# Optimization experiments

Measured on AMD Instinct MI355X. Metric: run time of the kernel, lower is better.

Reference implementation:

```python
import jax, jax.numpy as jnp
import numpy as np

B, C, H, W = 8, 128, 64, 64
GROUPS = 8
EPS = 1e-5


def setup_inputs() -> dict:
    key = jax.random.key(0)
    ks = jax.random.split(key, 4)
    x = jax.random.normal(ks[0], (B, C, H, W), dtype=jnp.float32)
    gamma = jnp.ones((C,), jnp.float32)
    beta = jnp.zeros((C,), jnp.float32)
    w_qkv = jax.random.normal(ks[1], (3 * C, C), jnp.float32) * (C ** -0.5)
    b_qkv = jnp.zeros((3 * C,), jnp.float32)
    w_proj = jax.random.normal(ks[2], (C, C), jnp.float32) * (C ** -0.5)
    b_proj = jnp.zeros((C,), jnp.float32)
    return {"x": x, "gamma": gamma, "beta": beta, "w_qkv": w_qkv,
            "b_qkv": b_qkv, "w_proj": w_proj, "b_proj": b_proj}


def group_norm(x, gamma, beta):
    b, c, h, w = x.shape
    xg = x.reshape(b, GROUPS, c // GROUPS, h, w)
    mean = xg.mean(axis=(2, 3, 4), keepdims=True)
    var = xg.var(axis=(2, 3, 4), keepdims=True)
    xn = ((xg - mean) * jax.lax.rsqrt(var + EPS)).reshape(b, c, h, w)
    return xn * gamma[None, :, None, None] + beta[None, :, None, None]


def reference(x, gamma, beta, w_qkv, b_qkv, w_proj, b_proj):
    b, c, h, w = x.shape
    n = h * w
    hn = group_norm(x, gamma, beta)
    # 1x1 conv == channel matmul
    qkv = jnp.einsum('oc,bchw->bohw', w_qkv, hn) + b_qkv[None, :, None, None]
    q, k, v = jnp.split(qkv.reshape(b, 3 * c, n), 3, axis=1)  # each [b,c,n]
    attn = jax.nn.softmax(jnp.einsum('bci,bcj->bij', q, k) * (c ** -0.5), axis=-1)
    out = jnp.einsum('bij,bcj->bci', attn, v).reshape(b, c, h, w)
    proj = jnp.einsum('oc,bchw->bohw', w_proj, out) + b_proj[None, :, None, None]
    return x + proj
```

## Files before the change

kernel.cpp:

```cpp
#include <hip/hip_runtime.h>
#include <cstdint>

#define NB 8
#define NC 128
#define NPIX 4096
#define NGROUP 8
#define CPG 16
#define EPS_GN 1e-5f
#define QSCALE 0.12751879523604132f
#define NSPLIT 2
#define JTILES (NPIX / 64 / NSPLIT)

typedef __attribute__((ext_vector_type(8))) short short8;
typedef __attribute__((ext_vector_type(16))) float f32x16;

typedef __attribute__((address_space(1))) const void gvoid_t;
typedef __attribute__((address_space(3))) void svoid_t;

__device__ __forceinline__ unsigned packbf(float lo, float hi) {
  unsigned r;
  asm("v_cvt_pk_bf16_f32 %0, %1, %2" : "=v"(r) : "v"(lo), "v"(hi));
  return r;
}

__device__ __forceinline__ int swK(int row) {
  return ((row & 7) << 1) | ((row >> 3) & 1);
}

__global__ __launch_bounds__(256) void k_gn_stats(const float* __restrict__ x,
                                                  float* __restrict__ stats) {
  int blk = blockIdx.x;
  const float4* base = (const float4*)(x + (size_t)blk * CPG * NPIX);
  float s = 0.f, ss = 0.f;
  for (int i = threadIdx.x; i < CPG * NPIX / 4; i += 256) {
    float4 v = base[i];
    s  += v.x + v.y + v.z + v.w;
    ss += v.x * v.x + v.y * v.y + v.z * v.z + v.w * v.w;
  }
#pragma unroll
  for (int off = 32; off >= 1; off >>= 1) {
    s  += __shfl_down(s, off);
    ss += __shfl_down(ss, off);
  }
  __shared__ float red[8];
  int wid = threadIdx.x >> 6;
  if ((threadIdx.x & 63) == 0) { red[wid] = s; red[4 + wid] = ss; }
  __syncthreads();
  if (threadIdx.x == 0) {
    float S  = red[0] + red[1] + red[2] + red[3];
    float SS = red[4] + red[5] + red[6] + red[7];
    float mean = S * (1.f / (CPG * NPIX));
    float var  = SS * (1.f / (CPG * NPIX)) - mean * mean;
    stats[blk * 2]     = mean;
    stats[blk * 2 + 1] = rsqrtf(var + EPS_GN);
  }
}

__global__ __launch_bounds__(256) void k_qkv(const float* __restrict__ x,
                                             const float* __restrict__ stats,
                                             const float* __restrict__ gamma,
                                             const float* __restrict__ beta,
                                             const float* __restrict__ w,
                                             const float* __restrict__ bias,
                                             ushort* __restrict__ qT,
                                             ushort* __restrict__ kT,
                                             ushort* __restrict__ vB) {
  __shared__ ushort At[128 * 128];
  __shared__ ushort Bt[128 * 128];
  __shared__ float sArr[128], tArr[128], biasS[384];
  int b = blockIdx.x, pt = blockIdx.y;
  int p0 = pt * 128;
  int tid = threadIdx.x;
  if (tid < 128) {
    int g = tid >> 4;
    float mean = stats[(b * NGROUP + g) * 2];
    float rstd = stats[(b * NGROUP + g) * 2 + 1];
    float sc = rstd * gamma[tid];
    sArr[tid] = sc;
    tArr[tid] = beta[tid] - mean * sc;
  }
  for (int i = tid; i < 384; i += 256) biasS[i] = bias[i];
  __syncthreads();
  const float* xb = x + (size_t)b * NC * NPIX;
#pragma unroll
  for (int u = 0; u < 8; ++u) {
    int task = tid + u * 256;
    int p = task & 127, cc = task >> 7;
    int c0 = cc * 8;
    float v[8];
#pragma unroll
    for (int i = 0; i < 8; ++i)
      v[i] = sArr[c0 + i] * xb[(size_t)(c0 + i) * NPIX + p0 + p] + tArr[c0 + i];
    uint4 pk;
    pk.x = packbf(v[0], v[1]); pk.y = packbf(v[2], v[3]);
    pk.z = packbf(v[4], v[5]); pk.w = packbf(v[6], v[7]);
    *(uint4*)&Bt[((p << 4) + (cc ^ (p & 7))) << 3] = pk;
  }
  int lane = tid & 63, wv = tid >> 6;
  int lq = lane & 31, h = lane >> 5;

  for (int ot = 0; ot < 3; ++ot) {
    __syncthreads();
#pragma unroll
    for (int u = 0; u < 8; ++u) {
      int task = tid + u * 256;
      int o = task >> 4, cc = task & 15;
      const float* wp = w + ((size_t)(ot * 128 + o)) * 128 + cc * 8;
      float4 a = *(const float4*)wp;
      float4 bq = *(const float4*)(wp + 4);
      uint4 pk;
      pk.x = packbf(a.x, a.y);  pk.y = packbf(a.z, a.w);
      pk.z = packbf(bq.x, bq.y); pk.w = packbf(bq.z, bq.w);
      *(uint4*)&At[((o << 4) + (cc ^ (o & 7))) << 3] = pk;
    }
    __syncthreads();
    short8 af[8];
    int arow = wv * 32 + lq;
#pragma unroll
    for (int kk = 0; kk < 8; ++kk) {
      int ch = kk * 2 + h;
      af[kk] = *(const short8*)&At[((arow << 4) + (ch ^ (arow & 7))) << 3];
    }
#pragma unroll
    for (int np = 0; np < 2; ++np) {
      int nt0 = np * 2, nt1 = np * 2 + 1;
      int br0 = nt0 * 32 + lq, br1 = nt1 * 32 + lq;
      f32x16 a0, a1;
#pragma unroll
      for (int r = 0; r < 16; ++r) { a0[r] = 0.f; a1[r] = 0.f; }
      __builtin_amdgcn_s_setprio(1);
#pragma unroll
      for (int kk = 0; kk < 8; ++kk) {
        int ch = kk * 2 + h;
        short8 h0 = *(const short8*)&Bt[((br0 << 4) + (ch ^ (br0 & 7))) << 3];
        short8 h1 = *(const short8*)&Bt[((br1 << 4) + (ch ^ (br1 & 7))) << 3];
        a0 = __builtin_amdgcn_mfma_f32_32x32x16_bf16(af[kk], h0, a0, 0, 0, 0);
        a1 = __builtin_amdgcn_mfma_f32_32x32x16_bf16(af[kk], h1, a1, 0, 0, 0);
      }
      __builtin_amdgcn_s_setprio(0);
#pragma unroll
      for (int half = 0; half < 2; ++half) {
        f32x16& acc = half ? a1 : a0;
        int pg = p0 + (half ? nt1 : nt0) * 32 + lq;
        if (ot < 2) {
          ushort* dst = (ot == 0) ? qT : kT;
          float sc = (ot == 0) ? QSCALE : 1.0f;
#pragma unroll
          for (int g2 = 0; g2 < 4; ++g2) {
            int orow = wv * 32 + 4 * h + 8 * g2;
            uint2 st;
            st.x = packbf((acc[g2 * 4 + 0] + biasS[ot * 128 + orow + 0]) * sc,
                          (acc[g2 * 4 + 1] + biasS[ot * 128 + orow + 1]) * sc);
            st.y = packbf((acc[g2 * 4 + 2] + biasS[ot * 128 + orow + 2]) * sc,
                          (acc[g2 * 4 + 3] + biasS[ot * 128 + orow + 3]) * sc);
            *(uint2*)&dst[(((size_t)b << 12) + pg) * 128 + orow] = st;
          }
        } else {
#pragma unroll
          for (int r = 0; r < 16; ++r) {
            int orow = wv * 32 + (r & 3) + 8 * (r >> 2) + 4 * h;
            float vv = acc[r] + biasS[256 + orow];
            vB[((size_t)(b * 128 + orow) << 12) + pg] = (ushort)(packbf(vv, vv) & 0xffffu);
          }
        }
      }
    }
  }
}

__device__ __forceinline__ void stage_dma(const ushort* __restrict__ kT,
                                          const ushort* __restrict__ vB,
                                          ushort* lds, int bufsel, int b, int j0,
                                          int wid, int lane) {
  ushort* base = lds + bufsel * 16384;
#pragma unroll
  for (int u = 0; u < 4; ++u) {
    int g = u * 4 + wid;
    int id = g * 64 + lane;
    int row = id >> 4, ch = id & 15;
    const ushort* src = kT + (((size_t)b << 12) + j0 + row) * 128 + ((ch ^ swK(row)) << 3);
    ushort* dst = base + g * 512;
    __builtin_amdgcn_global_load_lds((gvoid_t*)src, (svoid_t*)dst, 16, 0, 0);
  }
#pragma unroll
  for (int u = 0; u < 4; ++u) {
    int g = u * 4 + wid;
    int id = g * 64 + lane;
    int row = id >> 3, ch = id & 7;
    const ushort* src = vB + (((size_t)(b * 128 + row)) << 12) + j0 + ((ch ^ (row & 7)) << 3);
    ushort* dst = base + 8192 + g * 512;
    __builtin_amdgcn_global_load_lds((gvoid_t*)src, (svoid_t*)dst, 16, 0, 0);
  }
}

__global__ __launch_bounds__(256, 2) void k_attn(const ushort* __restrict__ qT,
                                                 const ushort* __restrict__ kT,
                                                 const ushort* __restrict__ vB,
                                                 float* __restrict__ attP,
                                                 float2* __restrict__ mlv) {
  __shared__ ushort lds[32768];
  int tid = threadIdx.x;
  int b = blockIdx.x, qt = blockIdx.y, s = blockIdx.z;
  int wid = tid >> 6;
  int lane = tid & 63;
  int lq = lane & 31;
  int h = lane >> 5;
  int q0 = qt * 128 + wid * 32;
  int jbase = s * (NPIX / NSPLIT);

  short8 qf[8];
  const ushort* qp = qT + (((size_t)b << 12) + q0 + lq) * 128 + h * 8;
#pragma unroll
  for (int kk = 0; kk < 8; ++kk) qf[kk] = *(const short8*)(qp + kk * 16);

  f32x16 pacc[4];
#pragma unroll
  for (int nt = 0; nt < 4; ++nt)
#pragma unroll
    for (int r = 0; r < 16; ++r) pacc[nt][r] = 0.f;
  float m_run = -1e30f, l_run = 0.f;

  stage_dma(kT, vB, lds, 0, b, jbase, wid, lane);

  for (int t = 0; t < JTILES; ++t) {
    __syncthreads();
    if (t + 1 < JTILES)
      stage_dma(kT, vB, lds, (t + 1) & 1, b, jbase + ((t + 1) << 6), wid, lane);
    const ushort* cur = lds + (t & 1) * 16384;

    f32x16 s0, s1;
#pragma unroll
    for (int r = 0; r < 16; ++r) { s0[r] = 0.f; s1[r] = 0.f; }
    __builtin_amdgcn_s_setprio(1);
#pragma unroll
    for (int kk = 0; kk < 8; ++kk) {
      int ch = (kk << 1) + h;
      int r0 = lq;
      int r1 = 32 + lq;
      short8 kf0 = *(const short8*)&cur[((r0 << 4) + (ch ^ swK(r0))) << 3];
      short8 kf1 = *(const short8*)&cur[((r1 << 4) + (ch ^ swK(r1))) << 3];
      s0 = __builtin_amdgcn_mfma_f32_32x32x16_bf16(kf0, qf[kk], s0, 0, 0, 0);
      s1 = __builtin_amdgcn_mfma_f32_32x32x16_bf16(kf1, qf[kk], s1, 0, 0, 0);
    }
    __builtin_amdgcn_s_setprio(0);

    float tm[8];
#pragma unroll
    for (int r = 0; r < 8; ++r)
      tm[r] = fmaxf(fmaxf(s0[2 * r], s0[2 * r + 1]), fmaxf(s1[2 * r], s1[2 * r + 1]));
    float tmax = fmaxf(fmaxf(fmaxf(tm[0], tm[1]), fmaxf(tm[2], tm[3])),
                       fmaxf(fmaxf(tm[4], tm[5]), fmaxf(tm[6], tm[7])));
    tmax = fmaxf(tmax, __shfl_xor(tmax, 32));

    bool noresc = __all(tmax - m_run <= 8.f);
    float mcur = noresc ? m_run : fmaxf(m_run, tmax);

    float sum = 0.f;
#pragma unroll
    for (int r = 0; r < 16; ++r) { s0[r] = exp2f(s0[r] - mcur); sum += s0[r]; }
#pragma unroll
    for (int r = 0; r < 16; ++r) { s1[r] = exp2f(s1[r] - mcur); sum += s1[r]; }
    sum += __shfl_xor(sum, 32);

    if (noresc) {
      l_run += sum;
    } else {
      float alpha = exp2f(m_run - mcur);
      m_run = mcur;
      l_run = l_run * alpha + sum;
#pragma unroll
      for (int r = 0; r < 16; ++r) {
        int qr = (r & 3) + ((r >> 2) << 3) + (h << 2);
        float av = __shfl(alpha, qr);
        pacc[0][r] *= av; pacc[1][r] *= av; pacc[2][r] *= av; pacc[3][r] *= av;
      }
    }

    short8 pa[4];
#pragma unroll
    for (int kk = 0; kk < 4; ++kk) {
      float v0, v1, v2, v3, v4, v5, v6, v7;
      if (kk == 0)      { v0=s0[0];v1=s0[1];v2=s0[2];v3=s0[3];v4=s0[4];v5=s0[5];v6=s0[6];v7=s0[7]; }
      else if (kk == 1) { v0=s0[8];v1=s0[9];v2=s0[10];v3=s0[11];v4=s0[12];v5=s0[13];v6=s0[14];v7=s0[15]; }
      else if (kk == 2) { v0=s1[0];v1=s1[1];v2=s1[2];v3=s1[3];v4=s1[4];v5=s1[5];v6=s1[6];v7=s1[7]; }
      else              { v0=s1[8];v1=s1[9];v2=s1[10];v3=s1[11];v4=s1[12];v5=s1[13];v6=s1[14];v7=s1[15]; }
      unsigned P0a = packbf(v0, v1), P0b = packbf(v2, v3);
      unsigned P1a = packbf(v4, v5), P1b = packbf(v6, v7);
      unsigned sA = h ? P0a : P1a, sB = h ? P0b : P1b;
      unsigned rA = (unsigned)__shfl_xor((int)sA, 32);
      unsigned rB = (unsigned)__shfl_xor((int)sB, 32);
      uint4 wv;
      wv.x = h ? rA : P0a;  wv.y = h ? rB : P0b;
      wv.z = h ? P1a : rA;  wv.w = h ? P1b : rB;
      pa[kk] = __builtin_bit_cast(short8, wv);
    }

    __builtin_amdgcn_s_setprio(1);
#pragma unroll
    for (int nt = 0; nt < 4; ++nt) {
      int row = (nt << 5) + lq;
#pragma unroll
      for (int kk = 0; kk < 4; ++kk) {
        int ch = (kk << 1) + h;
        short8 vf = *(const short8*)&cur[8192 + (((row << 3) + (ch ^ (row & 7))) << 3)];
        pacc[nt] = __builtin_amdgcn_mfma_f32_32x32x16_bf16(pa[kk], vf, pacc[nt], 0, 0, 0);
      }
    }
    __builtin_amdgcn_s_setprio(0);
  }

  size_t sb = (size_t)(s * NB + b);
#pragma unroll
  for (int r = 0; r < 16; ++r) {
    int qr = (r & 3) + ((r >> 2) << 3) + (h << 2);
    size_t rowbase = (((sb << 12) + q0 + qr) << 7) + lq;
    attP[rowbase]      = pacc[0][r];
    attP[rowbase + 32] = pacc[1][r];
    attP[rowbase + 64] = pacc[2][r];
    attP[rowbase + 96] = pacc[3][r];
  }
  if (h == 0) {
    mlv[(sb << 12) + q0 + lq] = make_float2(m_run, l_run);
  }
}

__global__ __launch_bounds__(256) void k_proj(const float* __restrict__ x,
                                              const float* __restrict__ attP,
                                              const float2* __restrict__ mlv,
                                              const float* __restrict__ w,
                                              const float* __restrict__ bias,
                                              float* __restrict__ out) {
  __shared__ ushort At[128 * 128];
  __shared__ ushort Bt[128 * 128];
  __shared__ float c0s[128], c1s[128], biasS[128];
  int b = blockIdx.x, pt = blockIdx.y;
  int p0 = pt * 128;
  int tid = threadIdx.x;
  if (tid < 128) {
    float2 ml0 = mlv[(((size_t)b) << 12) + p0 + tid];
    float2 ml1 = mlv[(((size_t)(NB + b)) << 12) + p0 + tid];
    float M = fmaxf(ml0.x, ml1.x);
    float e0 = exp2f(ml0.x - M), e1 = exp2f(ml1.x - M);
    float inv = 1.f / (ml0.y * e0 + ml1.y * e1);
    c0s[tid] = e0 * inv;
    c1s[tid] = e1 * inv;
    biasS[tid] = bias[tid];
  }
  __syncthreads();
#pragma unroll
  for (int u = 0; u < 8; ++u) {
    int task = tid + u * 256;
    int p = task & 127, cc = task >> 7;
    const float* a0 = attP + ((((size_t)b << 12) + p0 + p) << 7) + cc * 8;
    const float* a1 = attP + ((((size_t)(NB + b) << 12) + p0 + p) << 7) + cc * 8;
    float c0 = c0s[p], c1 = c1s[p];
    float v[8];
    float4 x0 = *(const float4*)a0, x0b = *(const float4*)(a0 + 4);
    float4 x1 = *(const float4*)a1, x1b = *(const float4*)(a1 + 4);
    v[0] = x0.x * c0 + x1.x * c1;  v[1] = x0.y * c0 + x1.y * c1;
    v[2] = x0.z * c0 + x1.z * c1;  v[3] = x0.w * c0 + x1.w * c1;
    v[4] = x0b.x * c0 + x1b.x * c1; v[5] = x0b.y * c0 + x1b.y * c1;
    v[6] = x0b.z * c0 + x1b.z * c1; v[7] = x0b.w * c0 + x1b.w * c1;
    uint4 pk;
    pk.x = packbf(v[0], v[1]); pk.y = packbf(v[2], v[3]);
    pk.z = packbf(v[4], v[5]); pk.w = packbf(v[6], v[7]);
    *(uint4*)&Bt[((p << 4) + (cc ^ (p & 7))) << 3] = pk;
  }
#pragma unroll
  for (int u = 0; u < 8; ++u) {
    int task = tid + u * 256;
    int o = task >> 4, cc = task & 15;
    const float* wp = w + (size_t)o * 128 + cc * 8;
    float4 a = *(const float4*)wp;
    float4 bq = *(const float4*)(wp + 4);
    uint4 pk;
    pk.x = packbf(a.x, a.y);  pk.y = packbf(a.z, a.w);
    pk.z = packbf(bq.x, bq.y); pk.w = packbf(bq.z, bq.w);
    *(uint4*)&At[((o << 4) + (cc ^ (o & 7))) << 3] = pk;
  }
  __syncthreads();
  int lane = tid & 63, wv = tid >> 6;
  int lq = lane & 31, h = lane >> 5;
  short8 af[8];
  int arow = wv * 32 + lq;
#pragma unroll
  for (int kk = 0; kk < 8; ++kk) {
    int ch = kk * 2 + h;
    af[kk] = *(const short8*)&At[((arow << 4) + (ch ^ (arow & 7))) << 3];
  }
  const float* xb = x + (size_t)b * NC * NPIX;
  float* ob = out + (size_t)b * NC * NPIX;
#pragma unroll
  for (int np = 0; np < 2; ++np) {
    int nt0 = np * 2, nt1 = np * 2 + 1;
    int br0 = nt0 * 32 + lq, br1 = nt1 * 32 + lq;
    f32x16 a0, a1;
#pragma unroll
    for (int r = 0; r < 16; ++r) { a0[r] = 0.f; a1[r] = 0.f; }
    __builtin_amdgcn_s_setprio(1);
#pragma unroll
    for (int kk = 0; kk < 8; ++kk) {
      int ch = kk * 2 + h;
      short8 h0 = *(const short8*)&Bt[((br0 << 4) + (ch ^ (br0 & 7))) << 3];
      short8 h1 = *(const short8*)&Bt[((br1 << 4) + (ch ^ (br1 & 7))) << 3];
      a0 = __builtin_amdgcn_mfma_f32_32x32x16_bf16(af[kk], h0, a0, 0, 0, 0);
      a1 = __builtin_amdgcn_mfma_f32_32x32x16_bf16(af[kk], h1, a1, 0, 0, 0);
    }
    __builtin_amdgcn_s_setprio(0);
#pragma unroll
    for (int half = 0; half < 2; ++half) {
      f32x16& acc = half ? a1 : a0;
      int pg = p0 + (half ? nt1 : nt0) * 32 + lq;
#pragma unroll
      for (int r = 0; r < 16; ++r) {
        int orow = wv * 32 + (r & 3) + 8 * (r >> 2) + 4 * h;
        size_t idx = ((size_t)orow << 12) + pg;
        ob[idx] = acc[r] + biasS[orow] + xb[idx];
      }
    }
  }
}

extern "C" void kernel_launch(void* const* d_in, const int* in_sizes, int n_in,
                              void* d_out, int out_size, void* d_ws, size_t ws_size,
                              hipStream_t stream) {
  const float* x      = (const float*)d_in[0];
  const float* gamma  = (const float*)d_in[1];
  const float* beta   = (const float*)d_in[2];
  const float* w_qkv  = (const float*)d_in[3];
  const float* b_qkv  = (const float*)d_in[4];
  const float* w_proj = (const float*)d_in[5];
  const float* b_proj = (const float*)d_in[6];
  float* out = (float*)d_out;
  char* wsb = (char*)d_ws;

  float*  stats  = (float*)wsb;
  ushort* qT     = (ushort*)(wsb + 1024);
  ushort* kT     = (ushort*)(wsb + 1024 + (8u << 20));
  ushort* vB     = (ushort*)(wsb + 1024 + (16u << 20));
  float*  attP   = (float*)(wsb + 1024 + (24u << 20));
  float2* mlv    = (float2*)(wsb + 1024 + (56u << 20));

  hipLaunchKernelGGL(k_gn_stats, dim3(NB * NGROUP), dim3(256), 0, stream, x, stats);
  hipLaunchKernelGGL(k_qkv, dim3(NB, NPIX / 128), dim3(256), 0, stream,
                     x, stats, gamma, beta, w_qkv, b_qkv, qT, kT, vB);
  hipLaunchKernelGGL(k_attn, dim3(NB, NPIX / 128, NSPLIT), dim3(256), 0, stream,
                     qT, kT, vB, attP, mlv);
  hipLaunchKernelGGL(k_proj, dim3(NB, NPIX / 128), dim3(256), 0, stream,
                     x, attP, mlv, w_proj, b_proj, out);
}
```

Baseline: 147.4 us.

## Switch attention kernel to 16x16x32 MFMA with 8 waves per block

The attention kernel now uses 512 threads (8 waves), each wave owning 16 query rows instead of 32, and switches from 32x32x16 to 16x16x32 bf16 MFMAs with rearranged fragment loads, reductions and P-matrix shuffles. DMA staging is split across 8 waves. This aims to cut per-wave register pressure and raise occupancy so more waves can hide LDS and MFMA latency. In exchange, each wave issues more LDS reads per MFMA and needs extra cross-lane shuffles to repack P.

```diff
diff --git a/kernel.cpp b/kernel.cpp
--- a/kernel.cpp
+++ b/kernel.cpp
@@ -12,6 +12,7 @@
 #define JTILES (NPIX / 64 / NSPLIT)
 
 typedef __attribute__((ext_vector_type(8))) short short8;
+typedef __attribute__((ext_vector_type(4))) float f32x4;
 typedef __attribute__((ext_vector_type(16))) float f32x16;
 
 typedef __attribute__((address_space(1))) const void gvoid_t;
@@ -174,8 +175,8 @@
                                           int wid, int lane) {
   ushort* base = lds + bufsel * 16384;
 #pragma unroll
-  for (int u = 0; u < 4; ++u) {
-    int g = u * 4 + wid;
+  for (int u = 0; u < 2; ++u) {
+    int g = u * 8 + wid;
     int id = g * 64 + lane;
     int row = id >> 4, ch = id & 15;
     const ushort* src = kT + (((size_t)b << 12) + j0 + row) * 128 + ((ch ^ swK(row)) << 3);
@@ -183,8 +184,8 @@
     __builtin_amdgcn_global_load_lds((gvoid_t*)src, (svoid_t*)dst, 16, 0, 0);
   }
 #pragma unroll
-  for (int u = 0; u < 4; ++u) {
-    int g = u * 4 + wid;
+  for (int u = 0; u < 2; ++u) {
+    int g = u * 8 + wid;
     int id = g * 64 + lane;
     int row = id >> 3, ch = id & 7;
     const ushort* src = vB + (((size_t)(b * 128 + row)) << 12) + j0 + ((ch ^ (row & 7)) << 3);
@@ -193,7 +194,7 @@
   }
 }
 
-__global__ __launch_bounds__(256, 2) void k_attn(const ushort* __restrict__ qT,
+__global__ __launch_bounds__(512, 4) void k_attn(const ushort* __restrict__ qT,
                                                  const ushort* __restrict__ kT,
                                                  const ushort* __restrict__ vB,
                                                  float* __restrict__ attP,
@@ -203,21 +204,21 @@
   int b = blockIdx.x, qt = blockIdx.y, s = blockIdx.z;
   int wid = tid >> 6;
   int lane = tid & 63;
-  int lq = lane & 31;
-  int h = lane >> 5;
-  int q0 = qt * 128 + wid * 32;
+  int lq = lane & 15;
+  int g = lane >> 4;
+  int q0 = qt * 128 + wid * 16;
   int jbase = s * (NPIX / NSPLIT);
 
-  short8 qf[8];
-  const ushort* qp = qT + (((size_t)b << 12) + q0 + lq) * 128 + h * 8;
-#pragma unroll
-  for (int kk = 0; kk < 8; ++kk) qf[kk] = *(const short8*)(qp + kk * 16);
-
-  f32x16 pacc[4];
-#pragma unroll
-  for (int nt = 0; nt < 4; ++nt)
-#pragma unroll
-    for (int r = 0; r < 16; ++r) pacc[nt][r] = 0.f;
+  short8 qf[4];
+  const ushort* qp = qT + (((size_t)b << 12) + q0 + lq) * 128 + g * 8;
+#pragma unroll
+  for (int kk = 0; kk < 4; ++kk) qf[kk] = *(const short8*)(qp + kk * 32);
+
+  f32x4 pacc[8];
+#pragma unroll
+  for (int ct = 0; ct < 8; ++ct)
+#pragma unroll
+    for (int r = 0; r < 4; ++r) pacc[ct][r] = 0.f;
   float m_run = -1e30f, l_run = 0.f;
 
   stage_dma(kT, vB, lds, 0, b, jbase, wid, lane);
@@ -228,28 +229,30 @@
       stage_dma(kT, vB, lds, (t + 1) & 1, b, jbase + ((t + 1) << 6), wid, lane);
     const ushort* cur = lds + (t & 1) * 16384;
 
-    f32x16 s0, s1;
-#pragma unroll
-    for (int r = 0; r < 16; ++r) { s0[r] = 0.f; s1[r] = 0.f; }
+    f32x4 sc[4];
+#pragma unroll
+    for (int jt = 0; jt < 4; ++jt)
+#pragma unroll
+      for (int r = 0; r < 4; ++r) sc[jt][r] = 0.f;
     __builtin_amdgcn_s_setprio(1);
 #pragma unroll
-    for (int kk = 0; kk < 8; ++kk) {
-      int ch = (kk << 1) + h;
-      int r0 = lq;
-      int r1 = 32 + lq;
-      short8 kf0 = *(const short8*)&cur[((r0 << 4) + (ch ^ swK(r0))) << 3];
-      short8 kf1 = *(const short8*)&cur[((r1 << 4) + (ch ^ swK(r1))) << 3];
-      s0 = __builtin_amdgcn_mfma_f32_32x32x16_bf16(kf0, qf[kk], s0, 0, 0, 0);
-      s1 = __builtin_amdgcn_mfma_f32_32x32x16_bf16(kf1, qf[kk], s1, 0, 0, 0);
+    for (int kk = 0; kk < 4; ++kk) {
+      int ch = kk * 4 + g;
+#pragma unroll
+      for (int jt = 0; jt < 4; ++jt) {
+        int row = jt * 16 + lq;
+        short8 kf = *(const short8*)&cur[((row << 4) + (ch ^ swK(row))) << 3];
+        sc[jt] = __builtin_amdgcn_mfma_f32_16x16x32_bf16(kf, qf[kk], sc[jt], 0, 0, 0);
+      }
     }
     __builtin_amdgcn_s_setprio(0);
 
-    float tm[8];
-#pragma unroll
-    for (int r = 0; r < 8; ++r)
-      tm[r] = fmaxf(fmaxf(s0[2 * r], s0[2 * r + 1]), fmaxf(s1[2 * r], s1[2 * r + 1]));
-    float tmax = fmaxf(fmaxf(fmaxf(tm[0], tm[1]), fmaxf(tm[2], tm[3])),
-                       fmaxf(fmaxf(tm[4], tm[5]), fmaxf(tm[6], tm[7])));
+    float tm0 = fmaxf(fmaxf(sc[0][0], sc[0][1]), fmaxf(sc[0][2], sc[0][3]));
+    float tm1 = fmaxf(fmaxf(sc[1][0], sc[1][1]), fmaxf(sc[1][2], sc[1][3]));
+    float tm2 = fmaxf(fmaxf(sc[2][0], sc[2][1]), fmaxf(sc[2][2], sc[2][3]));
+    float tm3 = fmaxf(fmaxf(sc[3][0], sc[3][1]), fmaxf(sc[3][2], sc[3][3]));
+    float tmax = fmaxf(fmaxf(tm0, tm1), fmaxf(tm2, tm3));
+    tmax = fmaxf(tmax, __shfl_xor(tmax, 16));
     tmax = fmaxf(tmax, __shfl_xor(tmax, 32));
 
     bool noresc = __all(tmax - m_run <= 8.f);
@@ -257,9 +260,13 @@
 
     float sum = 0.f;
 #pragma unroll
-    for (int r = 0; r < 16; ++r) { s0[r] = exp2f(s0[r] - mcur); sum += s0[r]; }
-#pragma unroll
-    for (int r = 0; r < 16; ++r) { s1[r] = exp2f(s1[r] - mcur); sum += s1[r]; }
+    for (int ft = 0; ft < 4; ++ft)
+#pragma unroll
+      for (int r = 0; r < 4; ++r) {
+        sc[ft][r] = exp2f(sc[ft][r] - mcur);
+        sum += sc[ft][r];
+      }
+    sum += __shfl_xor(sum, 16);
     sum += __shfl_xor(sum, 32);
 
     if (noresc) {
@@ -269,41 +276,44 @@
       m_run = mcur;
       l_run = l_run * alpha + sum;
 #pragma unroll
-      for (int r = 0; r < 16; ++r) {
-        int qr = (r & 3) + ((r >> 2) << 3) + (h << 2);
-        float av = __shfl(alpha, qr);
-        pacc[0][r] *= av; pacc[1][r] *= av; pacc[2][r] *= av; pacc[3][r] *= av;
-      }
-    }
-
-    short8 pa[4];
-#pragma unroll
-    for (int kk = 0; kk < 4; ++kk) {
-      float v0, v1, v2, v3, v4, v5, v6, v7;
-      if (kk == 0)      { v0=s0[0];v1=s0[1];v2=s0[2];v3=s0[3];v4=s0[4];v5=s0[5];v6=s0[6];v7=s0[7]; }
-      else if (kk == 1) { v0=s0[8];v1=s0[9];v2=s0[10];v3=s0[11];v4=s0[12];v5=s0[13];v6=s0[14];v7=s0[15]; }
-      else if (kk == 2) { v0=s1[0];v1=s1[1];v2=s1[2];v3=s1[3];v4=s1[4];v5=s1[5];v6=s1[6];v7=s1[7]; }
-      else              { v0=s1[8];v1=s1[9];v2=s1[10];v3=s1[11];v4=s1[12];v5=s1[13];v6=s1[14];v7=s1[15]; }
-      unsigned P0a = packbf(v0, v1), P0b = packbf(v2, v3);
-      unsigned P1a = packbf(v4, v5), P1b = packbf(v6, v7);
-      unsigned sA = h ? P0a : P1a, sB = h ? P0b : P1b;
-      unsigned rA = (unsigned)__shfl_xor((int)sA, 32);
-      unsigned rB = (unsigned)__shfl_xor((int)sB, 32);
+      for (int r = 0; r < 4; ++r) {
+        float av = __shfl(alpha, g * 4 + r);
+#pragma unroll
+        for (int ct = 0; ct < 8; ++ct) pacc[ct][r] *= av;
+      }
+    }
+
+    unsigned w0[4], w1[4];
+#pragma unroll
+    for (int ft = 0; ft < 4; ++ft) {
+      w0[ft] = packbf(sc[ft][0], sc[ft][1]);
+      w1[ft] = packbf(sc[ft][2], sc[ft][3]);
+    }
+    short8 pa[2];
+#pragma unroll
+    for (int kkp = 0; kkp < 2; ++kkp) {
+      unsigned wd[4];
+#pragma unroll
+      for (int s_ = 0; s_ < 4; ++s_) {
+        int src = lq + ((((g & 1) * 2) + (s_ >> 1)) << 4);
+        unsigned a0 = (unsigned)__shfl((int)((s_ & 1) ? w1[kkp * 2] : w0[kkp * 2]), src);
+        unsigned a1 = (unsigned)__shfl((int)((s_ & 1) ? w1[kkp * 2 + 1] : w0[kkp * 2 + 1]), src);
+        wd[s_] = (g >> 1) ? a1 : a0;
+      }
       uint4 wv;
-      wv.x = h ? rA : P0a;  wv.y = h ? rB : P0b;
-      wv.z = h ? P1a : rA;  wv.w = h ? P1b : rB;
-      pa[kk] = __builtin_bit_cast(short8, wv);
+      wv.x = wd[0]; wv.y = wd[1]; wv.z = wd[2]; wv.w = wd[3];
+      pa[kkp] = __builtin_bit_cast(short8, wv);
     }
 
     __builtin_amdgcn_s_setprio(1);
 #pragma unroll
-    for (int nt = 0; nt < 4; ++nt) {
-      int row = (nt << 5) + lq;
-#pragma unroll
-      for (int kk = 0; kk < 4; ++kk) {
-        int ch = (kk << 1) + h;
+    for (int kkp = 0; kkp < 2; ++kkp) {
+      int ch = kkp * 4 + g;
+#pragma unroll
+      for (int ct = 0; ct < 8; ++ct) {
+        int row = ct * 16 + lq;
         short8 vf = *(const short8*)&cur[8192 + (((row << 3) + (ch ^ (row & 7))) << 3)];
-        pacc[nt] = __builtin_amdgcn_mfma_f32_32x32x16_bf16(pa[kk], vf, pacc[nt], 0, 0, 0);
+        pacc[ct] = __builtin_amdgcn_mfma_f32_16x16x32_bf16(pa[kkp], vf, pacc[ct], 0, 0, 0);
       }
     }
     __builtin_amdgcn_s_setprio(0);
@@ -311,16 +321,14 @@
 
   size_t sb = (size_t)(s * NB + b);
 #pragma unroll
-  for (int r = 0; r < 16; ++r) {
-    int qr = (r & 3) + ((r >> 2) << 3) + (h << 2);
-    size_t rowbase = (((sb << 12) + q0 + qr) << 7) + lq;
-    attP[rowbase]      = pacc[0][r];
-    attP[rowbase + 32] = pacc[1][r];
-    attP[rowbase + 64] = pacc[2][r];
-    attP[rowbase + 96] = pacc[3][r];
-  }
-  if (h == 0) {
-    mlv[(sb << 12) + q0 + lq] = make_float2(m_run, l_run);
+  for (int ct = 0; ct < 8; ++ct)
+#pragma unroll
+    for (int r = 0; r < 4; ++r) {
+      int q = g * 4 + r;
+      attP[(((sb << 12) + q0 + q) << 7) + ct * 16 + lq] = pacc[ct][r];
+    }
+  if (lane < 16) {
+    mlv[(sb << 12) + q0 + lane] = make_float2(m_run, l_run);
   }
 }
 
@@ -444,7 +452,7 @@
   hipLaunchKernelGGL(k_gn_stats, dim3(NB * NGROUP), dim3(256), 0, stream, x, stats);
   hipLaunchKernelGGL(k_qkv, dim3(NB, NPIX / 128), dim3(256), 0, stream,
                      x, stats, gamma, beta, w_qkv, b_qkv, qT, kT, vB);
-  hipLaunchKernelGGL(k_attn, dim3(NB, NPIX / 128, NSPLIT), dim3(256), 0, stream,
+  hipLaunchKernelGGL(k_attn, dim3(NB, NPIX / 128, NSPLIT), dim3(512), 0, stream,
                      qT, kT, vB, attP, mlv);
   hipLaunchKernelGGL(k_proj, dim3(NB, NPIX / 128), dim3(256), 0, stream,
                      x, attP, mlv, w_proj, b_proj, out);
```

Measured after the change: 159.2 us. 1.08x slower.
